# Performance work log

Hardware: AMD Instinct MI355X
Metric: run time of the kernel (lower is better)

Reference implementation:

```python
import jax, jax.numpy as jnp
import numpy as np

B, N1, N2 = 16, 256, 256
FA, FE = 128, 128  # n_atom_feature, n_edge_feature


def setup_inputs() -> dict:
    key = jax.random.key(0)
    ks = jax.random.split(key, 8)
    x1 = jax.random.normal(ks[0], (B, N1, FA), dtype=jnp.float32)
    x2 = jax.random.normal(ks[1], (B, N2, FA), dtype=jnp.float32)
    edge = jax.random.normal(ks[2], (B, N1, N2, FE), dtype=jnp.float32)
    valid_edge = jax.random.randint(ks[3], (B, N1, N2), 0, 2).astype(jnp.float32)
    s_w = 1.0 / np.sqrt(FA)
    s_m = 1.0 / np.sqrt(FE + FA)
    W_w = jax.random.uniform(ks[4], (FA, FA), jnp.float32, -s_w, s_w)      # [in, out]
    W_b = jax.random.uniform(ks[5], (FA,), jnp.float32, -s_w, s_w)
    M_w = jax.random.uniform(ks[6], (FE + FA, FA), jnp.float32, -s_m, s_m)  # [in, out]
    M_b = jax.random.uniform(ks[7], (FA,), jnp.float32, -s_m, s_m)
    return {"x1": x1, "x2": x2, "edge": edge, "valid_edge": valid_edge,
            "W_w": W_w, "W_b": W_b, "M_w": M_w, "M_b": M_b}


def reference(x1, x2, edge, valid_edge, W_w, W_b, M_w, M_b):
    # m1 = W(x1): [B, N1, FA]
    m1 = jnp.einsum('bif,fg->big', x1, W_w) + W_b
    # M(new_edge) without materializing concat: split M into x2-part and edge-part.
    # new_edge = cat([broadcast(x2) -> [B,N1,N2,FA], edge], -1)
    Mw_x2 = M_w[:FA]    # [FA, FA]
    Mw_e = M_w[FA:]     # [FE, FA]
    me = jnp.einsum('bije,eg->bijg', edge, Mw_e)                 # [B,N1,N2,FA]
    mx2 = jnp.einsum('bjf,fg->bjg', x2, Mw_x2)                   # [B,N2,FA]
    m_edge = me + mx2[:, None, :, :] + M_b                       # [B,N1,N2,FA]
    # mask-multiply then max over neighbor axis (axis=2), as in the original
    m2 = jnp.max(m_edge * valid_edge[..., None], axis=2)         # [B,N1,FA]
    return jax.nn.relu(m1 + m2)
```

## Files before the change

kernel.cpp:

```cpp
#include <hip/hip_runtime.h>
#include <hip/hip_bf16.h>

#define BB 16
#define N1 256
#define N2 256
#define FA 128
#define FE 128

typedef __attribute__((ext_vector_type(8))) short bf16x8;
typedef __attribute__((ext_vector_type(4))) float f32x4;

static __device__ __forceinline__ unsigned short f2bf(float f) {
    union { float f; unsigned int u; } v; v.f = f;
    unsigned int u = v.u;
    unsigned int r = (u + 0x7FFFu + ((u >> 16) & 1u)) >> 16;
    return (unsigned short)r;
}

static __device__ __forceinline__ bf16x8 pack8(float4 lo, float4 hi) {
    bf16x8 r;
    r[0] = (short)f2bf(lo.x); r[1] = (short)f2bf(lo.y);
    r[2] = (short)f2bf(lo.z); r[3] = (short)f2bf(lo.w);
    r[4] = (short)f2bf(hi.x); r[5] = (short)f2bf(hi.y);
    r[6] = (short)f2bf(hi.z); r[7] = (short)f2bf(hi.w);
    return r;
}

__global__ __launch_bounds__(128) void prep_all(
    const float* __restrict__ x1, const float* __restrict__ x2,
    const float* __restrict__ W_w, const float* __restrict__ W_b,
    const float* __restrict__ M_w, const float* __restrict__ M_b,
    float* __restrict__ out, float* __restrict__ mx2bT,
    unsigned short* __restrict__ wT) {
    const int blk = blockIdx.x;
    const int g = threadIdx.x;

    if (blk >= 1024) {
        const int idx = (blk - 1024) * 128 + g;
        const int gg = idx >> 7, e = idx & 127;
        wT[idx] = f2bf(M_w[(size_t)(FA + e) * FA + gg]);
        return;
    }

    __shared__ float xs[8][128];
    const bool isT = (blk >= 512);
    const int r0 = (isT ? blk - 512 : blk) * 8;
    const float* x = isT ? x2 : x1;
    const float* W = isT ? M_w : W_w;
    const float* bias = isT ? M_b : W_b;

    #pragma unroll
    for (int r = 0; r < 8; ++r)
        xs[r][g] = x[(size_t)(r0 + r) * FA + g];
    __syncthreads();
    float acc[8];
    const float bv = bias[g];
    #pragma unroll
    for (int r = 0; r < 8; ++r) acc[r] = bv;
    #pragma unroll 8
    for (int f = 0; f < 128; ++f) {
        const float wv = W[f * FA + g];
        #pragma unroll
        for (int r = 0; r < 8; ++r) acc[r] += xs[r][f] * wv;
    }
    if (!isT) {
        #pragma unroll
        for (int r = 0; r < 8; ++r)
            out[(size_t)(r0 + r) * FA + g] = acc[r];
    } else {
        const int b = r0 >> 8, j0 = r0 & 255;
        float4 v0 = {acc[0], acc[1], acc[2], acc[3]};
        float4 v1 = {acc[4], acc[5], acc[6], acc[7]};
        float4* dst = (float4*)&mx2bT[(size_t)(b * 128 + g) * 256 + j0];
        dst[0] = v0;
        dst[1] = v1;
    }
}

__global__ __launch_bounds__(256, 4) void edge_main(
    const float* __restrict__ edge,
    const float* __restrict__ valid,
    const float* __restrict__ mx2bT,
    const unsigned short* __restrict__ wT,
    float* __restrict__ out)
{
    __shared__ __align__(16) unsigned short ebuf[2][4096];

    const int tid = threadIdx.x;
    const int wv = tid >> 6;
    const int lane = tid & 63;
    const int n = lane & 15, q = lane >> 4;
    const int bi = blockIdx.x;
    const int b = bi >> 8;

    bf16x8 bF0[4], bF1[4];
    #pragma unroll
    for (int s = 0; s < 4; ++s) {
        bF0[s] = *(const bf16x8*)&wT[((wv * 2 + 0) * 16 + n) * FE + s * 32 + q * 8];
        bF1[s] = *(const bf16x8*)&wT[((wv * 2 + 1) * 16 + n) * FE + s * 32 + q * 8];
    }

    const float* eb  = edge + (size_t)bi * (N2 * FE);
    const float* mxT = mx2bT + (size_t)b * (N2 * FA);
    const float* vb  = valid + (size_t)bi * N2;

    const int sj = tid >> 4;
    const int se = (tid & 15) * 8;
    const float* sg = eb + (size_t)sj * FE + se;
    char* ebase = (char*)&ebuf[0][0];
    const int sw = (sj & 7) << 4;
    const int sbyte0 = sj * 256 + (tid & 15) * 16;
    const int sp0 = sbyte0 ^ sw;
    const int sp1 = (4096 + sbyte0) ^ sw;

    {
        float4 a0 = *(const float4*)(sg);
        float4 a1 = *(const float4*)(sg + 4);
        float4 b0 = *(const float4*)(sg + 16 * FE);
        float4 b1 = *(const float4*)(sg + 16 * FE + 4);
        *(bf16x8*)(ebase + sp0) = pack8(a0, a1);
        *(bf16x8*)(ebase + sp1) = pack8(b0, b1);
    }
    __syncthreads();

    float runmax0 = -3.0e38f, runmax1 = -3.0e38f;
    const int lqb = n * 256 + q * 16;
    const int xsw = (n & 7) << 4;

    for (int strip = 0; strip < 8; ++strip) {
        const bool more = (strip + 1) < 8;
        const int j0 = strip * 32;

        float4 pa0, pa1, pb0, pb1;
        if (more) {
            const float* ns = sg + (size_t)(j0 + 32) * FE;
            pa0 = *(const float4*)(ns);
            pa1 = *(const float4*)(ns + 4);
            pb0 = *(const float4*)(ns + 16 * FE);
            pb1 = *(const float4*)(ns + 16 * FE + 4);
        }

        char* cbuf = ebase + (strip & 1) * 8192;

        #pragma unroll
        for (int h = 0; h < 2; ++h) {
            const int jh = j0 + h * 16;
            const float4 vld = *(const float4*)(vb + jh + q * 4);
            const float4 mxv0 = *(const float4*)(mxT + (size_t)((wv * 2 + 0) * 16 + n) * N2 + jh + q * 4);
            const float4 mxv1 = *(const float4*)(mxT + (size_t)((wv * 2 + 1) * 16 + n) * N2 + jh + q * 4);

            bf16x8 aF[4];
            #pragma unroll
            for (int s = 0; s < 4; ++s)
                aF[s] = *(const bf16x8*)(cbuf + ((h * 4096 + lqb + s * 64) ^ xsw));

            f32x4 acc0 = {0.f, 0.f, 0.f, 0.f};
            f32x4 acc1 = {0.f, 0.f, 0.f, 0.f};
            #pragma unroll
            for (int s = 0; s < 4; ++s) {
                acc0 = __builtin_amdgcn_mfma_f32_16x16x32_bf16(aF[s], bF0[s], acc0, 0, 0, 0);
                acc1 = __builtin_amdgcn_mfma_f32_16x16x32_bf16(aF[s], bF1[s], acc1, 0, 0, 0);
            }
            {
                float v0 = (acc0[0] + mxv0.x) * vld.x;
                float v1 = (acc0[1] + mxv0.y) * vld.y;
                float v2 = (acc0[2] + mxv0.z) * vld.z;
                float v3 = (acc0[3] + mxv0.w) * vld.w;
                runmax0 = fmaxf(runmax0, fmaxf(fmaxf(v0, v1), fmaxf(v2, v3)));
            }
            {
                float v0 = (acc1[0] + mxv1.x) * vld.x;
                float v1 = (acc1[1] + mxv1.y) * vld.y;
                float v2 = (acc1[2] + mxv1.z) * vld.z;
                float v3 = (acc1[3] + mxv1.w) * vld.w;
                runmax1 = fmaxf(runmax1, fmaxf(fmaxf(v0, v1), fmaxf(v2, v3)));
            }
        }

        if (more) {
            char* obuf = ebase + ((strip + 1) & 1) * 8192;
            *(bf16x8*)(obuf + sp0) = pack8(pa0, pa1);
            *(bf16x8*)(obuf + sp1) = pack8(pb0, pb1);
            __syncthreads();
        }
    }

    {
        float m = runmax0;
        m = fmaxf(m, __shfl_xor(m, 16, 64));
        m = fmaxf(m, __shfl_xor(m, 32, 64));
        if (lane < 16) {
            const size_t o = (size_t)bi * FA + (wv * 2 + 0) * 16 + lane;
            out[o] = fmaxf(out[o] + m, 0.0f);
        }
    }
    {
        float m = runmax1;
        m = fmaxf(m, __shfl_xor(m, 16, 64));
        m = fmaxf(m, __shfl_xor(m, 32, 64));
        if (lane < 16) {
            const size_t o = (size_t)bi * FA + (wv * 2 + 1) * 16 + lane;
            out[o] = fmaxf(out[o] + m, 0.0f);
        }
    }
}

extern "C" void kernel_launch(void* const* d_in, const int* in_sizes, int n_in,
                              void* d_out, int out_size, void* d_ws, size_t ws_size,
                              hipStream_t stream) {
    const float* x1    = (const float*)d_in[0];
    const float* x2    = (const float*)d_in[1];
    const float* edge  = (const float*)d_in[2];
    const float* valid = (const float*)d_in[3];
    const float* W_w   = (const float*)d_in[4];
    const float* W_b   = (const float*)d_in[5];
    const float* M_w   = (const float*)d_in[6];
    const float* M_b   = (const float*)d_in[7];
    float* out = (float*)d_out;

    unsigned short* wT = (unsigned short*)d_ws;
    float* mx2bT = (float*)((char*)d_ws + 32768);

    prep_all<<<1152, 128, 0, stream>>>(x1, x2, W_w, W_b, M_w, M_b, out, mx2bT, wT);
    edge_main<<<BB * N1, 256, 0, stream>>>(edge, valid, mx2bT, wT, out);
}
```

Baseline: 721.1 us.

## Prefetch edge strips two ahead with alternating register sets

The edge kernel's global-to-register prefetch now runs two strips ahead instead of one. It alternates between two register sets (P and Q) and fully unrolls the strip loop so the selection resolves at compile time. The goal is to keep more global loads in flight per wave, hiding memory latency in this bandwidth-bound reduction. The extra registers force the occupancy hint down from 4 to 3 blocks per CU, so there are fewer resident waves to hide latency with.

After: 727.9 us. About the same (+0.9%).

```diff
diff --git a/kernel.cpp b/kernel.cpp
--- a/kernel.cpp
+++ b/kernel.cpp
@@ -77,7 +77,7 @@
     }
 }
 
-__global__ __launch_bounds__(256, 4) void edge_main(
+__global__ __launch_bounds__(256, 3) void edge_main(
     const float* __restrict__ edge,
     const float* __restrict__ valid,
     const float* __restrict__ mx2bT,
@@ -108,58 +108,58 @@
     const int se = (tid & 15) * 8;
     const float* sg = eb + (size_t)sj * FE + se;
     char* ebase = (char*)&ebuf[0][0];
-    const int sw = (sj & 7) << 4;
-    const int sbyte0 = sj * 256 + (tid & 15) * 16;
-    const int sp0 = sbyte0 ^ sw;
-    const int sp1 = (4096 + sbyte0) ^ sw;
-
-    {
-        float4 a0 = *(const float4*)(sg);
-        float4 a1 = *(const float4*)(sg + 4);
-        float4 b0 = *(const float4*)(sg + 16 * FE);
-        float4 b1 = *(const float4*)(sg + 16 * FE + 4);
-        *(bf16x8*)(ebase + sp0) = pack8(a0, a1);
-        *(bf16x8*)(ebase + sp1) = pack8(b0, b1);
-    }
+    const int sb0 = (sj * 256 + (tid & 15) * 16) ^ ((sj & 7) << 4);
+    const int sb1 = sb0 + 4096;
+
+#define LDSTRIP(S, A0, A1, B0, B1)                                   \
+    {                                                                \
+        const float* p_ = sg + (size_t)(S) * 32 * FE;                \
+        A0 = *(const float4*)(p_);                                   \
+        A1 = *(const float4*)(p_ + 4);                               \
+        B0 = *(const float4*)(p_ + 16 * FE);                         \
+        B1 = *(const float4*)(p_ + 16 * FE + 4);                     \
+    }
+
+    float4 Pa0, Pa1, Pb0, Pb1, Qa0, Qa1, Qb0, Qb1;
+    LDSTRIP(0, Pa0, Pa1, Pb0, Pb1);
+    LDSTRIP(1, Qa0, Qa1, Qb0, Qb1);
+    *(bf16x8*)(ebase + sb0) = pack8(Pa0, Pa1);
+    *(bf16x8*)(ebase + sb1) = pack8(Pb0, Pb1);
     __syncthreads();
 
     float runmax0 = -3.0e38f, runmax1 = -3.0e38f;
     const int lqb = n * 256 + q * 16;
     const int xsw = (n & 7) << 4;
 
-    for (int strip = 0; strip < 8; ++strip) {
-        const bool more = (strip + 1) < 8;
-        const int j0 = strip * 32;
-
-        float4 pa0, pa1, pb0, pb1;
-        if (more) {
-            const float* ns = sg + (size_t)(j0 + 32) * FE;
-            pa0 = *(const float4*)(ns);
-            pa1 = *(const float4*)(ns + 4);
-            pb0 = *(const float4*)(ns + 16 * FE);
-            pb1 = *(const float4*)(ns + 16 * FE + 4);
-        }
-
-        char* cbuf = ebase + (strip & 1) * 8192;
-
+    #pragma unroll
+    for (int s = 0; s < 8; ++s) {
+        if (s + 2 < 8) {
+            if ((s & 1) == 0) {
+                LDSTRIP(s + 2, Pa0, Pa1, Pb0, Pb1);
+            } else {
+                LDSTRIP(s + 2, Qa0, Qa1, Qb0, Qb1);
+            }
+        }
+
+        char* cbuf = ebase + (s & 1) * 8192;
         #pragma unroll
         for (int h = 0; h < 2; ++h) {
-            const int jh = j0 + h * 16;
+            const int jh = s * 32 + h * 16;
             const float4 vld = *(const float4*)(vb + jh + q * 4);
             const float4 mxv0 = *(const float4*)(mxT + (size_t)((wv * 2 + 0) * 16 + n) * N2 + jh + q * 4);
             const float4 mxv1 = *(const float4*)(mxT + (size_t)((wv * 2 + 1) * 16 + n) * N2 + jh + q * 4);
 
             bf16x8 aF[4];
             #pragma unroll
-            for (int s = 0; s < 4; ++s)
-                aF[s] = *(const bf16x8*)(cbuf + ((h * 4096 + lqb + s * 64) ^ xsw));
+            for (int k = 0; k < 4; ++k)
+                aF[k] = *(const bf16x8*)(cbuf + ((h * 4096 + lqb + k * 64) ^ xsw));
 
             f32x4 acc0 = {0.f, 0.f, 0.f, 0.f};
             f32x4 acc1 = {0.f, 0.f, 0.f, 0.f};
             #pragma unroll
-            for (int s = 0; s < 4; ++s) {
-                acc0 = __builtin_amdgcn_mfma_f32_16x16x32_bf16(aF[s], bF0[s], acc0, 0, 0, 0);
-                acc1 = __builtin_amdgcn_mfma_f32_16x16x32_bf16(aF[s], bF1[s], acc1, 0, 0, 0);
+            for (int k = 0; k < 4; ++k) {
+                acc0 = __builtin_amdgcn_mfma_f32_16x16x32_bf16(aF[k], bF0[k], acc0, 0, 0, 0);
+                acc1 = __builtin_amdgcn_mfma_f32_16x16x32_bf16(aF[k], bF1[k], acc1, 0, 0, 0);
             }
             {
                 float v0 = (acc0[0] + mxv0.x) * vld.x;
@@ -177,13 +177,19 @@
             }
         }
 
-        if (more) {
-            char* obuf = ebase + ((strip + 1) & 1) * 8192;
-            *(bf16x8*)(obuf + sp0) = pack8(pa0, pa1);
-            *(bf16x8*)(obuf + sp1) = pack8(pb0, pb1);
+        if (s + 1 < 8) {
+            char* obuf = ebase + ((s + 1) & 1) * 8192;
+            if (((s + 1) & 1) == 0) {
+                *(bf16x8*)(obuf + sb0) = pack8(Pa0, Pa1);
+                *(bf16x8*)(obuf + sb1) = pack8(Pb0, Pb1);
+            } else {
+                *(bf16x8*)(obuf + sb0) = pack8(Qa0, Qa1);
+                *(bf16x8*)(obuf + sb1) = pack8(Qb0, Qb1);
+            }
             __syncthreads();
         }
     }
+#undef LDSTRIP
 
     {
         float m = runmax0;
```
